# Performance work log

Hardware: AMD Instinct MI355X
Metric: run time of the kernel (lower is better)

The kernel has to match this reference:

```python
import jax, jax.numpy as jnp
import numpy as np

N = 50000      # nodes
E = 800000     # edges (avg degree 16)
IN_DIM = 128
HIDDEN = 128
HEADS = 4
OUT = HIDDEN // HEADS  # 32 per-head out dim
NEG_SLOPE = 0.2        # DGL GATConv default leaky_relu slope


def setup_inputs() -> dict:
    key = jax.random.key(0)
    ks = jax.random.split(key, 12)
    x = jax.random.normal(ks[0], (N, IN_DIM), dtype=jnp.float32)
    src = jax.random.randint(ks[1], (E,), 0, N)
    dst = jax.random.randint(ks[2], (E,), 0, N)
    s = 0.1
    # layer 1 params
    W1 = jax.random.normal(ks[3], (IN_DIM, HEADS * OUT), dtype=jnp.float32) * s
    al1 = jax.random.normal(ks[4], (HEADS, OUT), dtype=jnp.float32) * s
    ar1 = jax.random.normal(ks[5], (HEADS, OUT), dtype=jnp.float32) * s
    b1 = jnp.zeros((HEADS * OUT,), dtype=jnp.float32)
    # layer 2 params (input = flattened heads of layer 1 = HIDDEN)
    W2 = jax.random.normal(ks[6], (HIDDEN, HEADS * OUT), dtype=jnp.float32) * s
    al2 = jax.random.normal(ks[7], (HEADS, OUT), dtype=jnp.float32) * s
    ar2 = jax.random.normal(ks[8], (HEADS, OUT), dtype=jnp.float32) * s
    b2 = jnp.zeros((HEADS * OUT,), dtype=jnp.float32)
    return {"x": x, "W1": W1, "al1": al1, "ar1": ar1, "b1": b1,
            "W2": W2, "al2": al2, "ar2": ar2, "b2": b2,
            "src": src, "dst": dst}


def gat_layer(x, W, a_l, a_r, b, src, dst):
    # x: [N, in], W: [in, H*D], a_l/a_r: [H, D], b: [H*D]
    z = (x @ W).reshape(N, HEADS, OUT)                # [N,H,D]
    el = jnp.sum(z * a_l[None], axis=-1)              # [N,H]
    er = jnp.sum(z * a_r[None], axis=-1)              # [N,H]
    e = jax.nn.leaky_relu(el[src] + er[dst], NEG_SLOPE)  # [E,H]
    # segment softmax over incoming edges of each dst node
    m = jax.ops.segment_max(e, dst, num_segments=N)   # [N,H]
    ex = jnp.exp(e - m[dst])                          # [E,H]
    s = jax.ops.segment_sum(ex, dst, num_segments=N)  # [N,H]
    alpha = ex / s[dst]                               # [E,H]
    out = jax.ops.segment_sum(z[src] * alpha[:, :, None], dst, num_segments=N)
    return out + b.reshape(1, HEADS, OUT)             # [N,H,D]


def reference(x, W1, al1, ar1, b1, W2, al2, ar2, b2, src, dst):
    # dropout is eval-mode (identity)
    h = gat_layer(x, W1, al1, ar1, b1, src, dst)      # [N,H,D]
    h = jax.nn.relu(h).reshape(N, HIDDEN)             # flatten heads between layers
    out = gat_layer(h, W2, al2, ar2, b2, src, dst)    # [N,H,D]
    return out
```

## Files before the change

### kernel.cpp

```cpp
#include <hip/hip_runtime.h>
#include <hip/hip_bf16.h>
#include <math.h>

#define N_NODES 50000
#define N_EDGES 800000
#define DIM 128
#define HEADS 4
#define CAP 64
#define NEG_SLOPE 0.2f
#define GEMM_BLKS 782
#define BUCKET_BLKS 3125

typedef __attribute__((ext_vector_type(8))) short bf16x8;
typedef __attribute__((ext_vector_type(4))) float f32x4;

__device__ __forceinline__ short f2bf_rne(float x) {
    __hip_bfloat16 h = __float2bfloat16(x);
    return *(short*)&h;
}
__device__ __forceinline__ float lrelu(float v) {
    return v > 0.f ? v : NEG_SLOPE * v;
}

__global__ __launch_bounds__(256) void prep_kernel(
    const float* __restrict__ W1, const float* __restrict__ W2,
    short* __restrict__ Wth, short* __restrict__ Wtl, int* __restrict__ cnt) {
    int t = blockIdx.x * blockDim.x + threadIdx.x;
    if (t < 2 * DIM * DIM) {
        int lay = t >> 14;
        int k = (t >> 7) & 127;
        int n = t & 127;
        float w = (lay ? W2 : W1)[k * DIM + n];
        int bits = __float_as_int(w);
        short hi = (short)(bits >> 16);
        float hif = __int_as_float(bits & 0xFFFF0000);
        short lo = f2bf_rne(w - hif);
        Wth[lay * DIM * DIM + n * DIM + k] = hi;
        Wtl[lay * DIM * DIM + n * DIM + k] = lo;
    }
    if (t < N_NODES) cnt[t] = 0;
}

__device__ __forceinline__ void gemm_eler_body(
    int blk, int tid,
    const float* __restrict__ X, const short* __restrict__ Wth,
    const short* __restrict__ Wtl, const float* __restrict__ al,
    const float* __restrict__ ar, short* __restrict__ Zb,
    float* __restrict__ el, float* __restrict__ er, int nrows) {
    int wv = tid >> 6, lane = tid & 63;
    int row0 = blk * 64 + wv * 16;
    int c = lane & 15;
    int g = lane >> 4;
    int rA = row0 + c;
    int rAc = rA < nrows ? rA : nrows - 1;
    int koff = g * 8;

    f32x4 acc[8];
#pragma unroll
    for (int n = 0; n < 8; ++n) acc[n] = (f32x4){0.f, 0.f, 0.f, 0.f};

#pragma unroll
    for (int ks = 0; ks < 4; ++ks) {
        int k0 = ks * 32 + koff;
        float4 xa = *(const float4*)&X[(size_t)rAc * DIM + k0];
        float4 xb = *(const float4*)&X[(size_t)rAc * DIM + k0 + 4];
        float xs[8] = {xa.x, xa.y, xa.z, xa.w, xb.x, xb.y, xb.z, xb.w};
        bf16x8 ah, alo;
#pragma unroll
        for (int j = 0; j < 8; ++j) {
            int bits = __float_as_int(xs[j]);
            ah[j] = (short)(bits >> 16);
            float hif = __int_as_float(bits & 0xFFFF0000);
            alo[j] = f2bf_rne(xs[j] - hif);
        }
#pragma unroll
        for (int n = 0; n < 8; ++n) {
            int ncol = n * 16 + c;
            bf16x8 bh = *(const bf16x8*)&Wth[ncol * DIM + k0];
            bf16x8 bl = *(const bf16x8*)&Wtl[ncol * DIM + k0];
            acc[n] = __builtin_amdgcn_mfma_f32_16x16x32_bf16(ah, bh, acc[n], 0, 0, 0);
            acc[n] = __builtin_amdgcn_mfma_f32_16x16x32_bf16(alo, bh, acc[n], 0, 0, 0);
            acc[n] = __builtin_amdgcn_mfma_f32_16x16x32_bf16(ah, bl, acc[n], 0, 0, 0);
        }
    }

    int rb = row0 + g * 4;
#pragma unroll
    for (int n = 0; n < 8; ++n) {
#pragma unroll
        for (int r = 0; r < 4; ++r) {
            int row = rb + r;
            if (row < nrows)
                Zb[(size_t)row * DIM + n * 16 + c] = f2bf_rne(acc[n][r]);
        }
    }

    f32x4 elv[4], erv[4];
#pragma unroll
    for (int r = 0; r < 4; ++r) { elv[r] = (f32x4){0,0,0,0}; erv[r] = (f32x4){0,0,0,0}; }
#pragma unroll
    for (int n = 0; n < 8; ++n) {
        int h = n >> 1;
        int idx = ((n & 1) << 4) + c;
        float av = al[h * 32 + idx];
        float bv = ar[h * 32 + idx];
#pragma unroll
        for (int r = 0; r < 4; ++r) {
            elv[r][h] += acc[n][r] * av;
            erv[r][h] += acc[n][r] * bv;
        }
    }
#pragma unroll
    for (int m = 1; m <= 8; m <<= 1) {
#pragma unroll
        for (int r = 0; r < 4; ++r) {
#pragma unroll
            for (int h = 0; h < 4; ++h) {
                elv[r][h] += __shfl_xor(elv[r][h], m);
                erv[r][h] += __shfl_xor(erv[r][h], m);
            }
        }
    }
    if (c < 4) {
        int row = rb + c;
        if (row < nrows) {
            f32x4 eo = c == 0 ? elv[0] : c == 1 ? elv[1] : c == 2 ? elv[2] : elv[3];
            f32x4 ro = c == 0 ? erv[0] : c == 1 ? erv[1] : c == 2 ? erv[2] : erv[3];
            *(float4*)&el[row * 4] = make_float4(eo[0], eo[1], eo[2], eo[3]);
            *(float4*)&er[row * 4] = make_float4(ro[0], ro[1], ro[2], ro[3]);
        }
    }
}

__global__ __launch_bounds__(256) void fused_gemm_bucket_kernel(
    const float* __restrict__ X, const short* __restrict__ Wth,
    const short* __restrict__ Wtl, const float* __restrict__ al,
    const float* __restrict__ ar, short* __restrict__ Zb,
    float* __restrict__ el, float* __restrict__ er,
    const int* __restrict__ src, const int* __restrict__ dst,
    int* __restrict__ cnt, int* __restrict__ srcs) {
    if (blockIdx.x < GEMM_BLKS) {
        gemm_eler_body(blockIdx.x, threadIdx.x, X, Wth, Wtl, al, ar, Zb, el, er, N_NODES);
    } else {
        int t = (blockIdx.x - GEMM_BLKS) * 256 + threadIdx.x;
        if (t < N_EDGES) {
            int d = dst[t];
            int pos = atomicAdd(&cnt[d], 1);
            if (pos < CAP) srcs[(d << 6) + pos] = src[t];
        }
    }
}

__global__ __launch_bounds__(256) void gemm_eler_kernel(
    const float* __restrict__ X, const short* __restrict__ Wth,
    const short* __restrict__ Wtl, const float* __restrict__ al,
    const float* __restrict__ ar, short* __restrict__ Zb,
    float* __restrict__ el, float* __restrict__ er) {
    gemm_eler_body(blockIdx.x, threadIdx.x, X, Wth, Wtl, al, ar, Zb, el, er, N_NODES);
}

__global__ __launch_bounds__(256) void csr_gat_kernel(
    const int* __restrict__ cnt, const int* __restrict__ srcs,
    const short* __restrict__ Zb, const float* __restrict__ el,
    const float* __restrict__ er, const float* __restrict__ b,
    float* __restrict__ out, int relu) {
    __shared__ float p_lds[4][4][64];
    __shared__ int   o_lds[4][64];
    int wv = threadIdx.x >> 6;
    int node = blockIdx.x * 4 + wv;
    int lane = threadIdx.x & 63;
    int h = lane >> 4;
    int d = cnt[node];
    d = d > CAP ? CAP : d;
    float4 er4 = *(const float4*)&er[node * HEADS];

    int s_reg = 0;
    float sv0 = 0.f, sv1 = 0.f, sv2 = 0.f, sv3 = 0.f;
    float mloc = -INFINITY;
    if (lane < d) {
        s_reg = srcs[(node << 6) + lane];
        float4 e4 = *(const float4*)&el[s_reg * HEADS];
        sv0 = lrelu(e4.x + er4.x); sv1 = lrelu(e4.y + er4.y);
        sv2 = lrelu(e4.z + er4.z); sv3 = lrelu(e4.w + er4.w);
        mloc = fmaxf(fmaxf(sv0, sv1), fmaxf(sv2, sv3));
    }
#pragma unroll
    for (int off = 32; off >= 1; off >>= 1)
        mloc = fmaxf(mloc, __shfl_xor(mloc, off));

    float p0 = 0.f, p1 = 0.f, p2 = 0.f, p3 = 0.f;
    if (lane < d) {
        p0 = __expf(sv0 - mloc); p1 = __expf(sv1 - mloc);
        p2 = __expf(sv2 - mloc); p3 = __expf(sv3 - mloc);
    }
    o_lds[wv][lane] = s_reg << 8;
    p_lds[wv][0][lane] = p0;
    p_lds[wv][1][lane] = p1;
    p_lds[wv][2][lane] = p2;
    p_lds[wv][3][lane] = p3;

    float ax = 0.f, ay = 0.f, sm = 0.f;
    const char* zbase = (const char*)Zb + lane * 4;
    int j = 0;
    for (; j + 4 <= d; j += 4) {
        int4 off4 = *(const int4*)&o_lds[wv][j];
        float4 p4 = *(const float4*)&p_lds[wv][h][j];
        int zz0 = *(const int*)(zbase + off4.x);
        int zz1 = *(const int*)(zbase + off4.y);
        int zz2 = *(const int*)(zbase + off4.z);
        int zz3 = *(const int*)(zbase + off4.w);
        ax += p4.x * __int_as_float(zz0 << 16);
        ay += p4.x * __int_as_float(zz0 & 0xFFFF0000);
        ax += p4.y * __int_as_float(zz1 << 16);
        ay += p4.y * __int_as_float(zz1 & 0xFFFF0000);
        ax += p4.z * __int_as_float(zz2 << 16);
        ay += p4.z * __int_as_float(zz2 & 0xFFFF0000);
        ax += p4.w * __int_as_float(zz3 << 16);
        ay += p4.w * __int_as_float(zz3 & 0xFFFF0000);
        sm += (p4.x + p4.y) + (p4.z + p4.w);
    }
    for (; j < d; ++j) {
        int off = o_lds[wv][j];
        float pv = p_lds[wv][h][j];
        int zz = *(const int*)(zbase + off);
        ax += pv * __int_as_float(zz << 16);
        ay += pv * __int_as_float(zz & 0xFFFF0000);
        sm += pv;
    }

    float inv = sm > 0.f ? 1.f / sm : 0.f;
    float2 bb = *(const float2*)&b[lane * 2];
    float ox = ax * inv + bb.x;
    float oy = ay * inv + bb.y;
    if (relu) { ox = fmaxf(ox, 0.f); oy = fmaxf(oy, 0.f); }
    *(float2*)&out[(size_t)node * DIM + lane * 2] = make_float2(ox, oy);
}

extern "C" void kernel_launch(void* const* d_in, const int* in_sizes, int n_in,
                              void* d_out, int out_size, void* d_ws, size_t ws_size,
                              hipStream_t stream) {
    const float* x   = (const float*)d_in[0];
    const float* W1  = (const float*)d_in[1];
    const float* al1 = (const float*)d_in[2];
    const float* ar1 = (const float*)d_in[3];
    const float* b1  = (const float*)d_in[4];
    const float* W2  = (const float*)d_in[5];
    const float* al2 = (const float*)d_in[6];
    const float* ar2 = (const float*)d_in[7];
    const float* b2  = (const float*)d_in[8];
    const int* src   = (const int*)d_in[9];
    const int* dst   = (const int*)d_in[10];

    char* ws = (char*)d_ws;
    float* h1   = (float*)ws; ws += (size_t)N_NODES * DIM * sizeof(float);
    short* Zb   = (short*)ws; ws += (size_t)N_NODES * DIM * sizeof(short);
    float* el   = (float*)ws; ws += (size_t)N_NODES * HEADS * sizeof(float);
    float* er   = (float*)ws; ws += (size_t)N_NODES * HEADS * sizeof(float);
    int*   cnt  = (int*)ws;   ws += (size_t)N_NODES * sizeof(int);
    int*   srcs = (int*)ws;   ws += (size_t)N_NODES * CAP * sizeof(int);
    short* Wth  = (short*)ws; ws += (size_t)2 * DIM * DIM * sizeof(short);
    short* Wtl  = (short*)ws; ws += (size_t)2 * DIM * DIM * sizeof(short);

    const int BLK = 256;
    int grid_prep = (N_NODES + BLK - 1) / BLK;
    int grid_gat  = N_NODES / 4;

    prep_kernel<<<grid_prep, BLK, 0, stream>>>(W1, W2, Wth, Wtl, cnt);
    fused_gemm_bucket_kernel<<<GEMM_BLKS + BUCKET_BLKS, BLK, 0, stream>>>(
        x, Wth, Wtl, al1, ar1, Zb, el, er, src, dst, cnt, srcs);
    csr_gat_kernel<<<grid_gat, BLK, 0, stream>>>(cnt, srcs, Zb, el, er, b1, h1, 1);
    gemm_eler_kernel<<<GEMM_BLKS, BLK, 0, stream>>>(h1, Wth + DIM * DIM, Wtl + DIM * DIM,
                                                    al2, ar2, Zb, el, er);
    csr_gat_kernel<<<grid_gat, BLK, 0, stream>>>(cnt, srcs, Zb, el, er, b2, (float*)d_out, 0);
}
```

Baseline: 177.4 us.

## Replace global-atomic edge bucketing with two-pass coarse/fine bucket sort

Edge bucketing by destination moves from per-edge global atomics into a scattered srcs array to a two-pass scheme. Pass one builds per-block shared-memory histograms over 64-node coarse buckets, reserves ranges with one global atomic per bucket, and writes (src,dst) pairs into h1 scratch. Pass two, fused with the first GEMM, sorts each coarse bucket into per-node slots in LDS and writes them out coalesced. This cuts global atomic contention and random writes, at the cost of an extra memset, an extra pass over the edges, and a per-bucket cap (CAPB) that could drop edges on skewed graphs.

```diff
diff --git a/kernel.cpp b/kernel.cpp
--- a/kernel.cpp
+++ b/kernel.cpp
@@ -9,7 +9,10 @@
 #define CAP 64
 #define NEG_SLOPE 0.2f
 #define GEMM_BLKS 782
-#define BUCKET_BLKS 3125
+#define NBUCK 782
+#define CAPB 1280
+#define P1_BLKS 100
+#define P1_EPB 8192
 
 typedef __attribute__((ext_vector_type(8))) short bf16x8;
 typedef __attribute__((ext_vector_type(4))) float f32x4;
@@ -22,23 +25,44 @@
     return v > 0.f ? v : NEG_SLOPE * v;
 }
 
-__global__ __launch_bounds__(256) void prep_kernel(
+__global__ __launch_bounds__(256) void prep_pass1_kernel(
     const float* __restrict__ W1, const float* __restrict__ W2,
-    short* __restrict__ Wth, short* __restrict__ Wtl, int* __restrict__ cnt) {
-    int t = blockIdx.x * blockDim.x + threadIdx.x;
-    if (t < 2 * DIM * DIM) {
-        int lay = t >> 14;
-        int k = (t >> 7) & 127;
-        int n = t & 127;
-        float w = (lay ? W2 : W1)[k * DIM + n];
-        int bits = __float_as_int(w);
-        short hi = (short)(bits >> 16);
-        float hif = __int_as_float(bits & 0xFFFF0000);
-        short lo = f2bf_rne(w - hif);
-        Wth[lay * DIM * DIM + n * DIM + k] = hi;
-        Wtl[lay * DIM * DIM + n * DIM + k] = lo;
-    }
-    if (t < N_NODES) cnt[t] = 0;
+    short* __restrict__ Wth, short* __restrict__ Wtl,
+    const int* __restrict__ src, const int* __restrict__ dst,
+    int* __restrict__ gcur, int2* __restrict__ pairs) {
+    if (blockIdx.x >= P1_BLKS) {
+        int t = (blockIdx.x - P1_BLKS) * 256 + threadIdx.x;
+        if (t < 2 * DIM * DIM) {
+            int lay = t >> 14;
+            int k = (t >> 7) & 127;
+            int n = t & 127;
+            float w = (lay ? W2 : W1)[k * DIM + n];
+            int bits = __float_as_int(w);
+            short hi = (short)(bits >> 16);
+            float hif = __int_as_float(bits & 0xFFFF0000);
+            Wth[lay * DIM * DIM + n * DIM + k] = hi;
+            Wtl[lay * DIM * DIM + n * DIM + k] = f2bf_rne(w - hif);
+        }
+        return;
+    }
+    __shared__ int hist[NBUCK], base_s[NBUCK], cur[NBUCK];
+    int tid = threadIdx.x;
+    for (int b = tid; b < NBUCK; b += 256) { hist[b] = 0; cur[b] = 0; }
+    __syncthreads();
+    int e0 = blockIdx.x * P1_EPB;
+    int e1 = e0 + P1_EPB; if (e1 > N_EDGES) e1 = N_EDGES;
+    for (int i = e0 + tid; i < e1; i += 256)
+        atomicAdd(&hist[dst[i] >> 6], 1);
+    __syncthreads();
+    for (int b = tid; b < NBUCK; b += 256)
+        if (hist[b]) base_s[b] = atomicAdd(&gcur[b], hist[b]);
+    __syncthreads();
+    for (int i = e0 + tid; i < e1; i += 256) {
+        int d = dst[i];
+        int b = d >> 6;
+        int pos = base_s[b] + atomicAdd(&cur[b], 1);
+        if (pos < CAPB) pairs[b * CAPB + pos] = make_int2(src[i], d);
+    }
 }
 
 __device__ __forceinline__ void gemm_eler_body(
@@ -132,22 +156,36 @@
     }
 }
 
-__global__ __launch_bounds__(256) void fused_gemm_bucket_kernel(
+__global__ __launch_bounds__(256) void fused_gemm_pass2_kernel(
     const float* __restrict__ X, const short* __restrict__ Wth,
     const short* __restrict__ Wtl, const float* __restrict__ al,
     const float* __restrict__ ar, short* __restrict__ Zb,
     float* __restrict__ el, float* __restrict__ er,
-    const int* __restrict__ src, const int* __restrict__ dst,
+    const int* __restrict__ gcur, const int2* __restrict__ pairs,
     int* __restrict__ cnt, int* __restrict__ srcs) {
     if (blockIdx.x < GEMM_BLKS) {
         gemm_eler_body(blockIdx.x, threadIdx.x, X, Wth, Wtl, al, ar, Zb, el, er, N_NODES);
     } else {
-        int t = (blockIdx.x - GEMM_BLKS) * 256 + threadIdx.x;
-        if (t < N_EDGES) {
-            int d = dst[t];
-            int pos = atomicAdd(&cnt[d], 1);
-            if (pos < CAP) srcs[(d << 6) + pos] = src[t];
-        }
+        __shared__ int lcnt[64];
+        __shared__ int fine[64 * CAP];
+        int b = blockIdx.x - GEMM_BLKS;
+        int tid = threadIdx.x;
+        if (tid < 64) lcnt[tid] = 0;
+        __syncthreads();
+        int ne = gcur[b]; if (ne > CAPB) ne = CAPB;
+        const int2* pb = pairs + b * CAPB;
+        for (int i = tid; i < ne; i += 256) {
+            int2 p = pb[i];
+            int ln = p.y & 63;
+            int pos = atomicAdd(&lcnt[ln], 1);
+            if (pos < CAP) fine[(ln << 6) + pos] = p.x;
+        }
+        __syncthreads();
+        int4* outp = (int4*)(srcs + ((size_t)b << 12));
+        const int4* f4 = (const int4*)fine;
+#pragma unroll
+        for (int i = 0; i < 4; ++i) outp[tid + i * 256] = f4[tid + i * 256];
+        if (tid < 64) cnt[b * 64 + tid] = lcnt[tid];
     }
 }
 
@@ -256,18 +294,21 @@
     short* Zb   = (short*)ws; ws += (size_t)N_NODES * DIM * sizeof(short);
     float* el   = (float*)ws; ws += (size_t)N_NODES * HEADS * sizeof(float);
     float* er   = (float*)ws; ws += (size_t)N_NODES * HEADS * sizeof(float);
-    int*   cnt  = (int*)ws;   ws += (size_t)N_NODES * sizeof(int);
-    int*   srcs = (int*)ws;   ws += (size_t)N_NODES * CAP * sizeof(int);
+    int*   cnt  = (int*)ws;   ws += (size_t)NBUCK * 64 * sizeof(int);
+    int*   srcs = (int*)ws;   ws += (size_t)NBUCK * 64 * CAP * sizeof(int);
     short* Wth  = (short*)ws; ws += (size_t)2 * DIM * DIM * sizeof(short);
     short* Wtl  = (short*)ws; ws += (size_t)2 * DIM * DIM * sizeof(short);
+    int*   gcur = (int*)ws;   ws += (size_t)NBUCK * sizeof(int);
+    int2*  pairs = (int2*)h1;
 
     const int BLK = 256;
-    int grid_prep = (N_NODES + BLK - 1) / BLK;
-    int grid_gat  = N_NODES / 4;
-
-    prep_kernel<<<grid_prep, BLK, 0, stream>>>(W1, W2, Wth, Wtl, cnt);
-    fused_gemm_bucket_kernel<<<GEMM_BLKS + BUCKET_BLKS, BLK, 0, stream>>>(
-        x, Wth, Wtl, al1, ar1, Zb, el, er, src, dst, cnt, srcs);
+    int grid_gat = N_NODES / 4;
+
+    hipMemsetAsync(gcur, 0, (size_t)NBUCK * sizeof(int), stream);
+    prep_pass1_kernel<<<P1_BLKS + 128, BLK, 0, stream>>>(W1, W2, Wth, Wtl,
+                                                         src, dst, gcur, pairs);
+    fused_gemm_pass2_kernel<<<GEMM_BLKS + NBUCK, BLK, 0, stream>>>(
+        x, Wth, Wtl, al1, ar1, Zb, el, er, gcur, pairs, cnt, srcs);
     csr_gat_kernel<<<grid_gat, BLK, 0, stream>>>(cnt, srcs, Zb, el, er, b1, h1, 1);
     gemm_eler_kernel<<<GEMM_BLKS, BLK, 0, stream>>>(h1, Wth + DIM * DIM, Wtl + DIM * DIM,
                                                     al2, ar2, Zb, el, er);
```

Measured after the change: 197.1 us. 1.11x slower.
